# Kernel optimization log

Measured on AMD Instinct MI355X. Metric: run time of the kernel, lower is better.

Reference implementation:

```python
import jax, jax.numpy as jnp
import numpy as np

B, T = 256, 64          # batch, rollout length
D, S, A, E, H = 1024, 64, 32, 1024, 1024  # deter, stoch, action, obs_embed, hidden


def setup_inputs() -> dict:
    key = jax.random.key(0)
    ks = jax.random.split(key, 12)
    f32 = jnp.float32

    def w(k, shape, fan_in):
        return (jax.random.normal(k, shape, f32) / np.float32(np.sqrt(fan_in)))

    return dict(
        obs_embeds=jax.random.normal(ks[0], (B, T, E), f32),
        action_embs=jax.random.normal(ks[1], (B, T, A), f32),
        noise_prior=jax.random.normal(ks[2], (T - 1, B, S), f32),  # randn_like in prior
        noise_post=jax.random.normal(ks[3], (T - 1, B, S), f32),   # randn_like in posterior
        # fc_state_action_embed: Linear(S+A -> D)
        W_sa=w(ks[4], (D, S + A), S + A), b_sa=jnp.zeros((D,), f32),
        # GRUCell(D, D): torch layout [3D, D] with gate order r, z, n
        W_ih=w(ks[5], (3 * D, D), D), b_ih=jnp.zeros((3 * D,), f32),
        W_hh=w(ks[6], (3 * D, D), D), b_hh=jnp.zeros((3 * D,), f32),
        # state_prior: Linear(D->H), ELU, Linear(H->2S)
        Wp1=w(ks[7], (H, D), D), bp1=jnp.zeros((H,), f32),
        Wp2=w(ks[8], (2 * S, H), H), bp2=jnp.zeros((2 * S,), f32),
        # state_posterior: Linear(D+E->H), ELU, Linear(H->2S)
        Wq1=w(ks[9], (H, D + E), D + E), bq1=jnp.zeros((H,), f32),
        Wq2=w(ks[10], (2 * S, H), H), bq2=jnp.zeros((2 * S,), f32),
    )


def reference(obs_embeds, action_embs, noise_prior, noise_post,
              W_sa, b_sa, W_ih, b_ih, W_hh, b_hh,
              Wp1, bp1, Wp2, bp2, Wq1, bq1, Wq2, bq2):
    # observe_rollout: init state is zeros; step t uses obs[:, t+1], action[:, t].
    b = obs_embeds.shape[0]
    h0 = jnp.zeros((b, D), obs_embeds.dtype)
    s0 = jnp.zeros((b, S), obs_embeds.dtype)
    obs_seq = jnp.swapaxes(obs_embeds[:, 1:], 0, 1)   # [T-1, B, E]
    act_seq = jnp.swapaxes(action_embs[:, :-1], 0, 1)  # [T-1, B, A]

    def step(carry, xs):
        h, s = carry  # posterior deter / stoch state from previous step
        obs, act, ep, eq = xs
        # prior: embed (stoch, action) -> GRU update
        e = jax.nn.elu(jnp.concatenate([s, act], -1) @ W_sa.T + b_sa)
        gi = e @ W_ih.T + b_ih
        gh = h @ W_hh.T + b_hh
        ir, iz, ia = jnp.split(gi, 3, axis=-1)
        hr, hz, ha = jnp.split(gh, 3, axis=-1)
        r = jax.nn.sigmoid(ir + hr)
        z = jax.nn.sigmoid(iz + hz)
        n = jnp.tanh(ia + r * ha)
        h_new = (1.0 - z) * n + z * h  # prior deter state
        # prior dist + reparam sample
        pm = jax.nn.elu(h_new @ Wp1.T + bp1) @ Wp2.T + bp2
        pmean, pstd = jnp.split(pm, 2, axis=-1)
        pstd = jax.nn.softplus(pstd) + 0.1
        pstoch = pmean + pstd * ep
        # posterior dist + reparam sample (conditioned on h_new and obs)
        qm = jax.nn.elu(jnp.concatenate([h_new, obs], -1) @ Wq1.T + bq1) @ Wq2.T + bq2
        qmean, qstd = jnp.split(qm, 2, axis=-1)
        qstd = jax.nn.softplus(qstd) + 0.1
        qstoch = qmean + qstd * eq
        out = jnp.concatenate([h_new, pmean, pstd, pstoch, qmean, qstd, qstoch], -1)
        return (h_new, qstoch), out

    _, outs = jax.lax.scan(step, (h0, s0), (obs_seq, act_seq, noise_prior, noise_post))
    # outs: [T-1, B, D + 6S] = (prior deter, prior mean/std/stoch, post mean/std/stoch)
    return outs
```

## Files before the change

### kernel.cpp

```cpp
#include <hip/hip_runtime.h>

typedef __attribute__((ext_vector_type(8))) short short8;
typedef __attribute__((ext_vector_type(4))) float f32x4;

#define OSTEP (256*1408)

#define OFF_WIH  ((size_t)0)
#define OFF_WHH  ((size_t)3145728)
#define OFF_WP1  ((size_t)6291456)
#define OFF_WQ1  ((size_t)7340032)
#define OFF_WP2  ((size_t)9437184)
#define OFF_WQ2  ((size_t)9568256)
#define OFF_HBF0 ((size_t)9699328)
#define OFF_HBF1 ((size_t)9961472)
#define OFF_EBF  ((size_t)10223616)
#define OFF_P1E  ((size_t)10485760)
#define OFF_Q1E  ((size_t)10747904)
#define F32_BYTE_OFF ((size_t)22020096)

__device__ __forceinline__ unsigned short f2bf(float f){
  union { float f; unsigned u; } v; v.f = f;
  unsigned u = v.u;
  u += 0x7fffu + ((u >> 16) & 1u);
  return (unsigned short)(u >> 16);
}
__device__ __forceinline__ float sigf(float x){ return 1.0f/(1.0f+__expf(-x)); }
__device__ __forceinline__ float tanhf_(float x){
  float e = __expf(-2.0f*fabsf(x));
  float t = (1.0f-e)/(1.0f+e);
  return x>=0.f ? t : -t;
}
__device__ __forceinline__ float eluf(float x){ return x>0.f ? x : __expf(x)-1.0f; }
__device__ __forceinline__ float softplusf(float x){ return x>20.f ? x : log1pf(__expf(x)); }
__device__ __forceinline__ short8 ld8(const unsigned short* p){ return *(const short8*)p; }

__global__ void k_prep(const float* __restrict__ wih, const float* __restrict__ whh,
                       const float* __restrict__ wp1, const float* __restrict__ wq1,
                       const float* __restrict__ wp2, const float* __restrict__ wq2,
                       unsigned short* __restrict__ dst){
  size_t i4 = ((size_t)blockIdx.x*256 + threadIdx.x)*4;
  const size_t total = 9699328;
  if(i4 >= total) return;
  const float* src; size_t off;
  if(i4 < 3145728){ src=wih; off=0; }
  else if(i4 < 6291456){ src=whh; off=3145728; }
  else if(i4 < 7340032){ src=wp1; off=6291456; }
  else if(i4 < 9437184){ src=wq1; off=7340032; }
  else if(i4 < 9568256){ src=wp2; off=9437184; }
  else { src=wq2; off=9568256; }
  size_t j = i4 - off;
  float4 v = *(const float4*)(src + j);
  unsigned long long p = (unsigned long long)f2bf(v.x)
                       | ((unsigned long long)f2bf(v.y) << 16)
                       | ((unsigned long long)f2bf(v.z) << 32)
                       | ((unsigned long long)f2bf(v.w) << 48);
  *(unsigned long long*)(dst + i4) = p;
}

__global__ __launch_bounds__(384) void k_gru(
    const unsigned short* __restrict__ e_bf,
    const unsigned short* __restrict__ h_bf,
    const unsigned short* __restrict__ wih_bf,
    const unsigned short* __restrict__ whh_bf,
    const float* __restrict__ b_ih, const float* __restrict__ b_hh,
    const float* __restrict__ hprev, int hprev_ld,
    float* __restrict__ out_t,
    unsigned short* __restrict__ hnext_bf)
{
  int bx = blockIdx.x, by = blockIdx.y;
  int tid = threadIdx.x, w = tid >> 6, lane = tid & 63;
  int g = w % 3; bool isI = (w < 3);
  const unsigned short* A  = isI ? e_bf  : h_bf;
  const unsigned short* Bw = isI ? wih_bf : whh_bf;
  int brow = g*1024 + bx*32;
  int arow = by*32;
  int l15 = lane & 15, q8 = (lane >> 4)*8;

  f32x4 z4 = {0.f,0.f,0.f,0.f};
  f32x4 acc00=z4, acc01=z4, acc10=z4, acc11=z4;

  const unsigned short* pa0 = A  + (size_t)(arow + l15)*1024 + q8;
  const unsigned short* pa1 = pa0 + 16*1024;
  const unsigned short* pb0 = Bw + (size_t)(brow + l15)*1024 + q8;
  const unsigned short* pb1 = pb0 + 16*1024;

  #pragma unroll 4
  for(int kk=0; kk<1024; kk+=32){
    short8 a0 = ld8(pa0+kk), a1 = ld8(pa1+kk);
    short8 b0 = ld8(pb0+kk), b1 = ld8(pb1+kk);
    acc00 = __builtin_amdgcn_mfma_f32_16x16x32_bf16(a0,b0,acc00,0,0,0);
    acc01 = __builtin_amdgcn_mfma_f32_16x16x32_bf16(a0,b1,acc01,0,0,0);
    acc10 = __builtin_amdgcn_mfma_f32_16x16x32_bf16(a1,b0,acc10,0,0,0);
    acc11 = __builtin_amdgcn_mfma_f32_16x16x32_bf16(a1,b1,acc11,0,0,0);
  }

  __shared__ float sg[6][32][33];
  int rr = (lane>>4)*4;
  #pragma unroll
  for(int v=0; v<4; v++){
    sg[w][0 +rr+v][0 +l15] = acc00[v];
    sg[w][0 +rr+v][16+l15] = acc01[v];
    sg[w][16+rr+v][0 +l15] = acc10[v];
    sg[w][16+rr+v][16+l15] = acc11[v];
  }
  __syncthreads();

  for(int i=tid; i<1024; i+=384){
    int m = i>>5, n = i&31;
    int d = bx*32+n, b = by*32+m;
    float ir = sg[0][m][n] + b_ih[d];
    float iz = sg[1][m][n] + b_ih[1024+d];
    float ia = sg[2][m][n] + b_ih[2048+d];
    float hr = sg[3][m][n] + b_hh[d];
    float hz = sg[4][m][n] + b_hh[1024+d];
    float ha = sg[5][m][n] + b_hh[2048+d];
    float r = sigf(ir+hr), zz = sigf(iz+hz);
    float nn = tanhf_(ia + r*ha);
    float hold = hprev[(size_t)b*hprev_ld + d];
    float hnew = (1.f-zz)*nn + zz*hold;
    out_t[(size_t)b*1408 + d] = hnew;
    hnext_bf[(size_t)b*1024 + d] = f2bf(hnew);
  }
}

__global__ __launch_bounds__(256) void k_heads1(
    const unsigned short* __restrict__ hnew_bf,
    const float* __restrict__ obs, int tcol,
    const unsigned short* __restrict__ wp1_bf,
    const unsigned short* __restrict__ wq1_bf,
    const float* __restrict__ bp1, const float* __restrict__ bq1,
    unsigned short* __restrict__ p1e, unsigned short* __restrict__ q1e)
{
  int bx = blockIdx.x, by = blockIdx.y;
  bool isQ = (bx >= 32); int nt = bx & 31;
  int tid = threadIdx.x, w = tid>>6, lane = tid&63;
  int mi = w & 1, ni = w >> 1;
  int l15 = lane & 15, q8 = (lane>>4)*8;
  int arowg = by*32 + mi*16 + l15;
  int browg = nt*32 + ni*16 + l15;

  f32x4 acc = {0.f,0.f,0.f,0.f};
  const unsigned short* pa = hnew_bf + (size_t)arowg*1024 + q8;

  if(!isQ){
    const unsigned short* pb = wp1_bf + (size_t)browg*1024 + q8;
    #pragma unroll 4
    for(int kk=0; kk<1024; kk+=32){
      acc = __builtin_amdgcn_mfma_f32_16x16x32_bf16(ld8(pa+kk), ld8(pb+kk), acc,0,0,0);
    }
  } else {
    const unsigned short* pb = wq1_bf + (size_t)browg*2048 + q8;
    #pragma unroll 4
    for(int kk=0; kk<1024; kk+=32){
      acc = __builtin_amdgcn_mfma_f32_16x16x32_bf16(ld8(pa+kk), ld8(pb+kk), acc,0,0,0);
    }
    const float* obsrow = obs + ((size_t)arowg*64 + tcol)*1024 + q8;
    #pragma unroll 4
    for(int kk=0; kk<1024; kk+=32){
      const float4* f = (const float4*)(obsrow + kk);
      float4 x0 = f[0], x1 = f[1];
      short8 a;
      a[0]=(short)f2bf(x0.x); a[1]=(short)f2bf(x0.y); a[2]=(short)f2bf(x0.z); a[3]=(short)f2bf(x0.w);
      a[4]=(short)f2bf(x1.x); a[5]=(short)f2bf(x1.y); a[6]=(short)f2bf(x1.z); a[7]=(short)f2bf(x1.w);
      acc = __builtin_amdgcn_mfma_f32_16x16x32_bf16(a, ld8(pb+1024+kk), acc,0,0,0);
    }
  }

  const float* bias = isQ ? bq1 : bp1;
  unsigned short* dst = isQ ? q1e : p1e;
  int col = browg;
  float bv = bias[col];
  #pragma unroll
  for(int v=0; v<4; v++){
    int b = by*32 + mi*16 + (lane>>4)*4 + v;
    float val = eluf(acc[v] + bv);
    dst[(size_t)b*1024 + col] = f2bf(val);
  }
}

__global__ __launch_bounds__(256) void k_heads2(
    const unsigned short* __restrict__ p1e, const unsigned short* __restrict__ q1e,
    const unsigned short* __restrict__ wp2_bf, const unsigned short* __restrict__ wq2_bf,
    const float* __restrict__ bp2, const float* __restrict__ bq2,
    float* __restrict__ pm, float* __restrict__ qm)
{
  int bx = blockIdx.x, by = blockIdx.y;
  int col0 = bx*32; bool isQ = (col0 >= 128); int c0 = col0 & 127;
  int tid = threadIdx.x, w = tid>>6, lane = tid&63;
  int mi = w & 1, ni = w >> 1;
  int l15 = lane & 15, q8 = (lane>>4)*8;
  const unsigned short* A  = isQ ? q1e : p1e;
  const unsigned short* Bw = isQ ? wq2_bf : wp2_bf;
  const float* bias = isQ ? bq2 : bp2;
  float* outb = isQ ? qm : pm;

  int arowg = by*32 + mi*16 + l15;
  int browg = c0 + ni*16 + l15;
  f32x4 acc = {0.f,0.f,0.f,0.f};
  const unsigned short* pa = A  + (size_t)arowg*1024 + q8;
  const unsigned short* pb = Bw + (size_t)browg*1024 + q8;
  #pragma unroll 4
  for(int kk=0; kk<1024; kk+=32){
    acc = __builtin_amdgcn_mfma_f32_16x16x32_bf16(ld8(pa+kk), ld8(pb+kk), acc,0,0,0);
  }
  float bv = bias[browg];
  #pragma unroll
  for(int v=0; v<4; v++){
    int b = by*32 + mi*16 + (lane>>4)*4 + v;
    outb[(size_t)b*128 + browg] = acc[v] + bv;
  }
}

__global__ __launch_bounds__(256) void k_sample_e(
    int t_out, int t_act,
    const float* __restrict__ pm, const float* __restrict__ qm,
    const float* __restrict__ noise_p, const float* __restrict__ noise_q,
    const float* __restrict__ act, const float* __restrict__ w_sa,
    const float* __restrict__ b_sa,
    float* __restrict__ out, unsigned short* __restrict__ e_bf)
{
  __shared__ float qst[32*64];
  __shared__ float sact[32*32];
  int bx = blockIdx.x, by = blockIdx.y, tid = threadIdx.x;

  if(t_out >= 0){
    float* out_t = out + (size_t)t_out*OSTEP;
    for(int i=tid; i<2048; i+=256){
      int m = i>>6, s = i&63; int b = by*32+m;
      float qmean = qm[(size_t)b*128 + s];
      float qstd  = softplusf(qm[(size_t)b*128 + 64 + s]) + 0.1f;
      float qs = qmean + qstd * noise_q[((size_t)t_out*256 + b)*64 + s];
      qst[m*64+s] = qs;
      if(bx == 0){
        float pmean = pm[(size_t)b*128 + s];
        float pstd  = softplusf(pm[(size_t)b*128 + 64 + s]) + 0.1f;
        float ps = pmean + pstd * noise_p[((size_t)t_out*256 + b)*64 + s];
        float* o = out_t + (size_t)b*1408;
        o[1024+s] = pmean; o[1088+s] = pstd; o[1152+s] = ps;
        o[1216+s] = qmean; o[1280+s] = qstd; o[1344+s] = qs;
      }
    }
  } else {
    for(int i=tid; i<2048; i+=256) qst[i] = 0.f;
  }
  for(int i=tid; i<1024; i+=256){
    int m = i>>5, k = i&31;
    sact[i] = act[((size_t)(by*32+m)*64 + t_act)*32 + k];
  }
  __syncthreads();

  int n = tid & 31, mb = tid >> 5;
  int d = bx*32 + n;
  const float* wrow = w_sa + (size_t)d*96;
  float a0=b_sa[d], a1=a0, a2=a0, a3=a0;
  for(int k=0; k<64; k++){
    float wv = wrow[k];
    a0 += qst[(mb+ 0)*64+k]*wv;
    a1 += qst[(mb+ 8)*64+k]*wv;
    a2 += qst[(mb+16)*64+k]*wv;
    a3 += qst[(mb+24)*64+k]*wv;
  }
  for(int k=0; k<32; k++){
    float wv = wrow[64+k];
    a0 += sact[(mb+ 0)*32+k]*wv;
    a1 += sact[(mb+ 8)*32+k]*wv;
    a2 += sact[(mb+16)*32+k]*wv;
    a3 += sact[(mb+24)*32+k]*wv;
  }
  e_bf[(size_t)(by*32+mb+ 0)*1024 + d] = f2bf(eluf(a0));
  e_bf[(size_t)(by*32+mb+ 8)*1024 + d] = f2bf(eluf(a1));
  e_bf[(size_t)(by*32+mb+16)*1024 + d] = f2bf(eluf(a2));
  e_bf[(size_t)(by*32+mb+24)*1024 + d] = f2bf(eluf(a3));
}

extern "C" void kernel_launch(void* const* d_in, const int* in_sizes, int n_in,
                              void* d_out, int out_size, void* d_ws, size_t ws_size,
                              hipStream_t stream) {
  const float* obs = (const float*)d_in[0];
  const float* act = (const float*)d_in[1];
  const float* np_ = (const float*)d_in[2];
  const float* nq_ = (const float*)d_in[3];
  const float* wsa = (const float*)d_in[4];
  const float* bsa = (const float*)d_in[5];
  const float* wih = (const float*)d_in[6];
  const float* bih = (const float*)d_in[7];
  const float* whh = (const float*)d_in[8];
  const float* bhh = (const float*)d_in[9];
  const float* wp1 = (const float*)d_in[10];
  const float* bp1 = (const float*)d_in[11];
  const float* wp2 = (const float*)d_in[12];
  const float* bp2 = (const float*)d_in[13];
  const float* wq1 = (const float*)d_in[14];
  const float* bq1 = (const float*)d_in[15];
  const float* wq2 = (const float*)d_in[16];
  const float* bq2 = (const float*)d_in[17];
  float* out = (float*)d_out;

  unsigned short* wsb = (unsigned short*)d_ws;
  unsigned short* wihb = wsb + OFF_WIH;
  unsigned short* whhb = wsb + OFF_WHH;
  unsigned short* wp1b = wsb + OFF_WP1;
  unsigned short* wq1b = wsb + OFF_WQ1;
  unsigned short* wp2b = wsb + OFF_WP2;
  unsigned short* wq2b = wsb + OFF_WQ2;
  unsigned short* hbf0 = wsb + OFF_HBF0;
  unsigned short* hbf1 = wsb + OFF_HBF1;
  unsigned short* ebf  = wsb + OFF_EBF;
  unsigned short* p1e  = wsb + OFF_P1E;
  unsigned short* q1e  = wsb + OFF_Q1E;
  float* f32b = (float*)((char*)d_ws + F32_BYTE_OFF);
  float* h0 = f32b;
  float* pm = f32b + 262144;
  float* qm = f32b + 262144 + 32768;

  hipMemsetAsync(hbf0, 0, 262144*2, stream);
  hipMemsetAsync(h0, 0, 262144*4, stream);

  k_prep<<<9472, 256, 0, stream>>>(wih, whh, wp1, wq1, wp2, wq2, wsb);

  k_sample_e<<<dim3(32,8), 256, 0, stream>>>(-1, 0, pm, qm, np_, nq_, act, wsa, bsa, out, ebf);

  for(int t=0; t<63; t++){
    const unsigned short* hb = (t&1) ? hbf1 : hbf0;
    unsigned short* hbn      = (t&1) ? hbf0 : hbf1;
    const float* hprev = t ? (out + (size_t)(t-1)*OSTEP) : h0;
    int hld = t ? 1408 : 1024;
    k_gru<<<dim3(32,8), 384, 0, stream>>>(ebf, hb, wihb, whhb, bih, bhh,
                                          hprev, hld, out + (size_t)t*OSTEP, hbn);
    k_heads1<<<dim3(64,8), 256, 0, stream>>>(hbn, obs, t+1, wp1b, wq1b, bp1, bq1, p1e, q1e);
    k_heads2<<<dim3(8,8), 256, 0, stream>>>(p1e, q1e, wp2b, wq2b, bp2, bq2, pm, qm);
    k_sample_e<<<dim3(32,8), 256, 0, stream>>>(t, t+1, pm, qm, np_, nq_, act, wsa, bsa, out, ebf);
  }
}
```

Before: 5.991 ms.

## Replace per-step kernel launches with single persistent cooperative kernel using grid syncs

Replaces the prep plus four-kernels-per-timestep launch sequence with one persistent cooperative kernel of 256 blocks that loops over all 63 steps and separates phases with grid.sync. The GRU gates are fused into a single tile pass with all six accumulators per wave, and the obs slice is converted to bf16 once per step. The head-2 output, sampling and the state-action embedding are merged into one phase, with the embedding now done by MFMA in bf16. This removes about 250 kernel launches and the global round-trips for pm/qm, at the cost of grid-wide barriers, idle blocks in the smaller phases, and extra bf16 rounding in the embedding.

```diff
diff --git a/kernel.cpp b/kernel.cpp
--- a/kernel.cpp
+++ b/kernel.cpp
@@ -1,4 +1,7 @@
 #include <hip/hip_runtime.h>
+#include <hip/hip_cooperative_groups.h>
+
+namespace cg = cooperative_groups;
 
 typedef __attribute__((ext_vector_type(8))) short short8;
 typedef __attribute__((ext_vector_type(4))) float f32x4;
@@ -11,12 +14,13 @@
 #define OFF_WQ1  ((size_t)7340032)
 #define OFF_WP2  ((size_t)9437184)
 #define OFF_WQ2  ((size_t)9568256)
-#define OFF_HBF0 ((size_t)9699328)
-#define OFF_HBF1 ((size_t)9961472)
-#define OFF_EBF  ((size_t)10223616)
-#define OFF_P1E  ((size_t)10485760)
-#define OFF_Q1E  ((size_t)10747904)
-#define F32_BYTE_OFF ((size_t)22020096)
+#define OFF_WSA  ((size_t)9699328)
+#define OFF_HBF0 ((size_t)9797632)
+#define OFF_HBF1 ((size_t)10059776)
+#define OFF_EBF  ((size_t)10321920)
+#define OFF_P1E  ((size_t)10584064)
+#define OFF_Q1E  ((size_t)10846208)
+#define OFF_OBSB ((size_t)11108352)
 
 __device__ __forceinline__ unsigned short f2bf(float f){
   union { float f; unsigned u; } v; v.f = f;
@@ -24,6 +28,10 @@
   u += 0x7fffu + ((u >> 16) & 1u);
   return (unsigned short)(u >> 16);
 }
+__device__ __forceinline__ unsigned long long pack4(float4 v){
+  return (unsigned long long)f2bf(v.x) | ((unsigned long long)f2bf(v.y)<<16)
+       | ((unsigned long long)f2bf(v.z)<<32) | ((unsigned long long)f2bf(v.w)<<48);
+}
 __device__ __forceinline__ float sigf(float x){ return 1.0f/(1.0f+__expf(-x)); }
 __device__ __forceinline__ float tanhf_(float x){
   float e = __expf(-2.0f*fabsf(x));
@@ -33,244 +41,210 @@
 __device__ __forceinline__ float eluf(float x){ return x>0.f ? x : __expf(x)-1.0f; }
 __device__ __forceinline__ float softplusf(float x){ return x>20.f ? x : log1pf(__expf(x)); }
 __device__ __forceinline__ short8 ld8(const unsigned short* p){ return *(const short8*)p; }
-
-__global__ void k_prep(const float* __restrict__ wih, const float* __restrict__ whh,
-                       const float* __restrict__ wp1, const float* __restrict__ wq1,
-                       const float* __restrict__ wp2, const float* __restrict__ wq2,
-                       unsigned short* __restrict__ dst){
-  size_t i4 = ((size_t)blockIdx.x*256 + threadIdx.x)*4;
-  const size_t total = 9699328;
-  if(i4 >= total) return;
-  const float* src; size_t off;
-  if(i4 < 3145728){ src=wih; off=0; }
-  else if(i4 < 6291456){ src=whh; off=3145728; }
-  else if(i4 < 7340032){ src=wp1; off=6291456; }
-  else if(i4 < 9437184){ src=wq1; off=7340032; }
-  else if(i4 < 9568256){ src=wp2; off=9437184; }
-  else { src=wq2; off=9568256; }
-  size_t j = i4 - off;
-  float4 v = *(const float4*)(src + j);
-  unsigned long long p = (unsigned long long)f2bf(v.x)
-                       | ((unsigned long long)f2bf(v.y) << 16)
-                       | ((unsigned long long)f2bf(v.z) << 32)
-                       | ((unsigned long long)f2bf(v.w) << 48);
-  *(unsigned long long*)(dst + i4) = p;
-}
-
-__global__ __launch_bounds__(384) void k_gru(
-    const unsigned short* __restrict__ e_bf,
-    const unsigned short* __restrict__ h_bf,
-    const unsigned short* __restrict__ wih_bf,
-    const unsigned short* __restrict__ whh_bf,
-    const float* __restrict__ b_ih, const float* __restrict__ b_hh,
-    const float* __restrict__ hprev, int hprev_ld,
-    float* __restrict__ out_t,
-    unsigned short* __restrict__ hnext_bf)
+__device__ __forceinline__ short8 cvt8(const float* p){
+  short8 r;
+  #pragma unroll
+  for(int i=0;i<8;i++) r[i]=(short)f2bf(p[i]);
+  return r;
+}
+#define MFMA(a,b,c) __builtin_amdgcn_mfma_f32_16x16x32_bf16((a),(b),(c),0,0,0)
+
+__device__ __forceinline__ void e_gemm(int row0, int w, int lane,
+    const float (*sst)[96], const unsigned short* wsab, const float* bsa,
+    unsigned short* ebf){
+  int l15 = lane&15, q8 = (lane>>4)*8, rr = (lane>>4)*4;
+  short8 a0 = cvt8(&sst[l15][q8]);
+  short8 a1 = cvt8(&sst[l15][32+q8]);
+  short8 a2 = cvt8(&sst[l15][64+q8]);
+  #pragma unroll 4
+  for(int n=0;n<16;n++){
+    int col = w*256 + n*16 + l15;
+    const unsigned short* pb = wsab + (size_t)col*96 + q8;
+    f32x4 c = {0.f,0.f,0.f,0.f};
+    c = MFMA(a0, ld8(pb),    c);
+    c = MFMA(a1, ld8(pb+32), c);
+    c = MFMA(a2, ld8(pb+64), c);
+    float bb = bsa[col];
+    #pragma unroll
+    for(int v=0;v<4;v++)
+      ebf[(size_t)(row0+rr+v)*1024 + col] = f2bf(eluf(c[v]+bb));
+  }
+}
+
+__global__ __launch_bounds__(256,1) void k_rssm(
+    const float* __restrict__ obs, const float* __restrict__ act,
+    const float* __restrict__ np_, const float* __restrict__ nq_,
+    const float* __restrict__ wsa_f, const float* __restrict__ bsa,
+    const float* __restrict__ wih_f, const float* __restrict__ bih,
+    const float* __restrict__ whh_f, const float* __restrict__ bhh,
+    const float* __restrict__ wp1_f, const float* __restrict__ bp1,
+    const float* __restrict__ wp2_f, const float* __restrict__ bp2,
+    const float* __restrict__ wq1_f, const float* __restrict__ bq1,
+    const float* __restrict__ wq2_f, const float* __restrict__ bq2,
+    float* __restrict__ out, unsigned short* __restrict__ wsb)
 {
-  int bx = blockIdx.x, by = blockIdx.y;
-  int tid = threadIdx.x, w = tid >> 6, lane = tid & 63;
-  int g = w % 3; bool isI = (w < 3);
-  const unsigned short* A  = isI ? e_bf  : h_bf;
-  const unsigned short* Bw = isI ? wih_bf : whh_bf;
-  int brow = g*1024 + bx*32;
-  int arow = by*32;
-  int l15 = lane & 15, q8 = (lane >> 4)*8;
-
-  f32x4 z4 = {0.f,0.f,0.f,0.f};
-  f32x4 acc00=z4, acc01=z4, acc10=z4, acc11=z4;
-
-  const unsigned short* pa0 = A  + (size_t)(arow + l15)*1024 + q8;
-  const unsigned short* pa1 = pa0 + 16*1024;
-  const unsigned short* pb0 = Bw + (size_t)(brow + l15)*1024 + q8;
-  const unsigned short* pb1 = pb0 + 16*1024;
-
-  #pragma unroll 4
-  for(int kk=0; kk<1024; kk+=32){
-    short8 a0 = ld8(pa0+kk), a1 = ld8(pa1+kk);
-    short8 b0 = ld8(pb0+kk), b1 = ld8(pb1+kk);
-    acc00 = __builtin_amdgcn_mfma_f32_16x16x32_bf16(a0,b0,acc00,0,0,0);
-    acc01 = __builtin_amdgcn_mfma_f32_16x16x32_bf16(a0,b1,acc01,0,0,0);
-    acc10 = __builtin_amdgcn_mfma_f32_16x16x32_bf16(a1,b0,acc10,0,0,0);
-    acc11 = __builtin_amdgcn_mfma_f32_16x16x32_bf16(a1,b1,acc11,0,0,0);
-  }
-
-  __shared__ float sg[6][32][33];
-  int rr = (lane>>4)*4;
-  #pragma unroll
-  for(int v=0; v<4; v++){
-    sg[w][0 +rr+v][0 +l15] = acc00[v];
-    sg[w][0 +rr+v][16+l15] = acc01[v];
-    sg[w][16+rr+v][0 +l15] = acc10[v];
-    sg[w][16+rr+v][16+l15] = acc11[v];
-  }
-  __syncthreads();
-
-  for(int i=tid; i<1024; i+=384){
-    int m = i>>5, n = i&31;
-    int d = bx*32+n, b = by*32+m;
-    float ir = sg[0][m][n] + b_ih[d];
-    float iz = sg[1][m][n] + b_ih[1024+d];
-    float ia = sg[2][m][n] + b_ih[2048+d];
-    float hr = sg[3][m][n] + b_hh[d];
-    float hz = sg[4][m][n] + b_hh[1024+d];
-    float ha = sg[5][m][n] + b_hh[2048+d];
-    float r = sigf(ir+hr), zz = sigf(iz+hz);
-    float nn = tanhf_(ia + r*ha);
-    float hold = hprev[(size_t)b*hprev_ld + d];
-    float hnew = (1.f-zz)*nn + zz*hold;
-    out_t[(size_t)b*1408 + d] = hnew;
-    hnext_bf[(size_t)b*1024 + d] = f2bf(hnew);
-  }
-}
-
-__global__ __launch_bounds__(256) void k_heads1(
-    const unsigned short* __restrict__ hnew_bf,
-    const float* __restrict__ obs, int tcol,
-    const unsigned short* __restrict__ wp1_bf,
-    const unsigned short* __restrict__ wq1_bf,
-    const float* __restrict__ bp1, const float* __restrict__ bq1,
-    unsigned short* __restrict__ p1e, unsigned short* __restrict__ q1e)
-{
-  int bx = blockIdx.x, by = blockIdx.y;
-  bool isQ = (bx >= 32); int nt = bx & 31;
-  int tid = threadIdx.x, w = tid>>6, lane = tid&63;
-  int mi = w & 1, ni = w >> 1;
-  int l15 = lane & 15, q8 = (lane>>4)*8;
-  int arowg = by*32 + mi*16 + l15;
-  int browg = nt*32 + ni*16 + l15;
-
-  f32x4 acc = {0.f,0.f,0.f,0.f};
-  const unsigned short* pa = hnew_bf + (size_t)arowg*1024 + q8;
-
-  if(!isQ){
-    const unsigned short* pb = wp1_bf + (size_t)browg*1024 + q8;
-    #pragma unroll 4
-    for(int kk=0; kk<1024; kk+=32){
-      acc = __builtin_amdgcn_mfma_f32_16x16x32_bf16(ld8(pa+kk), ld8(pb+kk), acc,0,0,0);
-    }
-  } else {
-    const unsigned short* pb = wq1_bf + (size_t)browg*2048 + q8;
-    #pragma unroll 4
-    for(int kk=0; kk<1024; kk+=32){
-      acc = __builtin_amdgcn_mfma_f32_16x16x32_bf16(ld8(pa+kk), ld8(pb+kk), acc,0,0,0);
-    }
-    const float* obsrow = obs + ((size_t)arowg*64 + tcol)*1024 + q8;
-    #pragma unroll 4
-    for(int kk=0; kk<1024; kk+=32){
-      const float4* f = (const float4*)(obsrow + kk);
-      float4 x0 = f[0], x1 = f[1];
-      short8 a;
-      a[0]=(short)f2bf(x0.x); a[1]=(short)f2bf(x0.y); a[2]=(short)f2bf(x0.z); a[3]=(short)f2bf(x0.w);
-      a[4]=(short)f2bf(x1.x); a[5]=(short)f2bf(x1.y); a[6]=(short)f2bf(x1.z); a[7]=(short)f2bf(x1.w);
-      acc = __builtin_amdgcn_mfma_f32_16x16x32_bf16(a, ld8(pb+1024+kk), acc,0,0,0);
-    }
-  }
-
-  const float* bias = isQ ? bq1 : bp1;
-  unsigned short* dst = isQ ? q1e : p1e;
-  int col = browg;
-  float bv = bias[col];
-  #pragma unroll
-  for(int v=0; v<4; v++){
-    int b = by*32 + mi*16 + (lane>>4)*4 + v;
-    float val = eluf(acc[v] + bv);
-    dst[(size_t)b*1024 + col] = f2bf(val);
-  }
-}
-
-__global__ __launch_bounds__(256) void k_heads2(
-    const unsigned short* __restrict__ p1e, const unsigned short* __restrict__ q1e,
-    const unsigned short* __restrict__ wp2_bf, const unsigned short* __restrict__ wq2_bf,
-    const float* __restrict__ bp2, const float* __restrict__ bq2,
-    float* __restrict__ pm, float* __restrict__ qm)
-{
-  int bx = blockIdx.x, by = blockIdx.y;
-  int col0 = bx*32; bool isQ = (col0 >= 128); int c0 = col0 & 127;
-  int tid = threadIdx.x, w = tid>>6, lane = tid&63;
-  int mi = w & 1, ni = w >> 1;
-  int l15 = lane & 15, q8 = (lane>>4)*8;
-  const unsigned short* A  = isQ ? q1e : p1e;
-  const unsigned short* Bw = isQ ? wq2_bf : wp2_bf;
-  const float* bias = isQ ? bq2 : bp2;
-  float* outb = isQ ? qm : pm;
-
-  int arowg = by*32 + mi*16 + l15;
-  int browg = c0 + ni*16 + l15;
-  f32x4 acc = {0.f,0.f,0.f,0.f};
-  const unsigned short* pa = A  + (size_t)arowg*1024 + q8;
-  const unsigned short* pb = Bw + (size_t)browg*1024 + q8;
-  #pragma unroll 4
-  for(int kk=0; kk<1024; kk+=32){
-    acc = __builtin_amdgcn_mfma_f32_16x16x32_bf16(ld8(pa+kk), ld8(pb+kk), acc,0,0,0);
-  }
-  float bv = bias[browg];
-  #pragma unroll
-  for(int v=0; v<4; v++){
-    int b = by*32 + mi*16 + (lane>>4)*4 + v;
-    outb[(size_t)b*128 + browg] = acc[v] + bv;
-  }
-}
-
-__global__ __launch_bounds__(256) void k_sample_e(
-    int t_out, int t_act,
-    const float* __restrict__ pm, const float* __restrict__ qm,
-    const float* __restrict__ noise_p, const float* __restrict__ noise_q,
-    const float* __restrict__ act, const float* __restrict__ w_sa,
-    const float* __restrict__ b_sa,
-    float* __restrict__ out, unsigned short* __restrict__ e_bf)
-{
-  __shared__ float qst[32*64];
-  __shared__ float sact[32*32];
-  int bx = blockIdx.x, by = blockIdx.y, tid = threadIdx.x;
-
-  if(t_out >= 0){
-    float* out_t = out + (size_t)t_out*OSTEP;
-    for(int i=tid; i<2048; i+=256){
-      int m = i>>6, s = i&63; int b = by*32+m;
-      float qmean = qm[(size_t)b*128 + s];
-      float qstd  = softplusf(qm[(size_t)b*128 + 64 + s]) + 0.1f;
-      float qs = qmean + qstd * noise_q[((size_t)t_out*256 + b)*64 + s];
-      qst[m*64+s] = qs;
-      if(bx == 0){
-        float pmean = pm[(size_t)b*128 + s];
-        float pstd  = softplusf(pm[(size_t)b*128 + 64 + s]) + 0.1f;
-        float ps = pmean + pstd * noise_p[((size_t)t_out*256 + b)*64 + s];
-        float* o = out_t + (size_t)b*1408;
-        o[1024+s] = pmean; o[1088+s] = pstd; o[1152+s] = ps;
-        o[1216+s] = qmean; o[1280+s] = qstd; o[1344+s] = qs;
-      }
-    }
-  } else {
-    for(int i=tid; i<2048; i+=256) qst[i] = 0.f;
-  }
-  for(int i=tid; i<1024; i+=256){
-    int m = i>>5, k = i&31;
-    sact[i] = act[((size_t)(by*32+m)*64 + t_act)*32 + k];
-  }
-  __syncthreads();
-
-  int n = tid & 31, mb = tid >> 5;
-  int d = bx*32 + n;
-  const float* wrow = w_sa + (size_t)d*96;
-  float a0=b_sa[d], a1=a0, a2=a0, a3=a0;
-  for(int k=0; k<64; k++){
-    float wv = wrow[k];
-    a0 += qst[(mb+ 0)*64+k]*wv;
-    a1 += qst[(mb+ 8)*64+k]*wv;
-    a2 += qst[(mb+16)*64+k]*wv;
-    a3 += qst[(mb+24)*64+k]*wv;
-  }
-  for(int k=0; k<32; k++){
-    float wv = wrow[64+k];
-    a0 += sact[(mb+ 0)*32+k]*wv;
-    a1 += sact[(mb+ 8)*32+k]*wv;
-    a2 += sact[(mb+16)*32+k]*wv;
-    a3 += sact[(mb+24)*32+k]*wv;
-  }
-  e_bf[(size_t)(by*32+mb+ 0)*1024 + d] = f2bf(eluf(a0));
-  e_bf[(size_t)(by*32+mb+ 8)*1024 + d] = f2bf(eluf(a1));
-  e_bf[(size_t)(by*32+mb+16)*1024 + d] = f2bf(eluf(a2));
-  e_bf[(size_t)(by*32+mb+24)*1024 + d] = f2bf(eluf(a3));
+  cg::grid_group grid = cg::this_grid();
+  const int p = blockIdx.x, tid = threadIdx.x;
+  const int w = tid>>6, lane = tid&63;
+  const int l15 = lane&15, q8 = (lane>>4)*8, rr = (lane>>4)*4;
+  const int gtid = p*256 + tid;
+
+  unsigned short* wihb = wsb + OFF_WIH;
+  unsigned short* whhb = wsb + OFF_WHH;
+  unsigned short* wp1b = wsb + OFF_WP1;
+  unsigned short* wq1b = wsb + OFF_WQ1;
+  unsigned short* wp2b = wsb + OFF_WP2;
+  unsigned short* wq2b = wsb + OFF_WQ2;
+  unsigned short* wsab = wsb + OFF_WSA;
+  unsigned short* ebf  = wsb + OFF_EBF;
+  unsigned short* p1e  = wsb + OFF_P1E;
+  unsigned short* q1e  = wsb + OFF_Q1E;
+  unsigned short* obsb = wsb + OFF_OBSB;
+
+  __shared__ float sm[16][130];
+  __shared__ float sst[16][96];
+
+  {
+    const float* srcs[7] = {wih_f, whh_f, wp1_f, wq1_f, wp2_f, wq2_f, wsa_f};
+    const size_t offs[7] = {OFF_WIH, OFF_WHH, OFF_WP1, OFF_WQ1, OFF_WP2, OFF_WQ2, OFF_WSA};
+    const size_t cnts[7] = {3145728,3145728,1048576,2097152,131072,131072,98304};
+    #pragma unroll 1
+    for(int s=0;s<7;s++){
+      const float4* src = (const float4*)srcs[s];
+      unsigned long long* dst = (unsigned long long*)(wsb + offs[s]);
+      size_t n4 = cnts[s] >> 2;
+      for(size_t i=gtid; i<n4; i+=65536) dst[i] = pack4(src[i]);
+    }
+    unsigned long long* hz = (unsigned long long*)(wsb + OFF_HBF0);
+    hz[gtid] = 0ull;
+  }
+  grid.sync();
+
+  if(p < 16){
+    int row0 = p*16;
+    for(int i=tid;i<16*96;i+=256) (&sst[0][0])[i] = 0.f;
+    __syncthreads();
+    for(int i=tid;i<512;i+=256){ int r=i>>5, a2=i&31;
+      sst[r][64+a2] = act[((size_t)(row0+r)*64 + 0)*32 + a2]; }
+    __syncthreads();
+    e_gemm(row0, w, lane, sst, wsab, bsa, ebf);
+  }
+  grid.sync();
+
+  for(int t=0;t<63;t++){
+    const unsigned short* hb  = (t&1) ? wsb+OFF_HBF1 : wsb+OFF_HBF0;
+    unsigned short*       hbn = (t&1) ? wsb+OFF_HBF0 : wsb+OFF_HBF1;
+    float* out_t = out + (size_t)t*OSTEP;
+
+    {
+      int j = p>>2, m = p&3;
+      int row0 = m*64 + w*16;
+      const unsigned short* pe = ebf + (size_t)(row0+l15)*1024 + q8;
+      const unsigned short* ph = hb  + (size_t)(row0+l15)*1024 + q8;
+      int d = j*16 + l15;
+      const unsigned short* pwi = wihb + (size_t)d*1024 + q8;
+      const unsigned short* pwh = whhb + (size_t)d*1024 + q8;
+      f32x4 z4 = {0.f,0.f,0.f,0.f};
+      f32x4 aIR=z4, aIZ=z4, aIA=z4, aHR=z4, aHZ=z4, aHA=z4;
+      #pragma unroll 2
+      for(int k=0;k<1024;k+=32){
+        short8 ae = ld8(pe+k), ah = ld8(ph+k);
+        aIR = MFMA(ae, ld8(pwi+k),         aIR);
+        aIZ = MFMA(ae, ld8(pwi+1048576+k), aIZ);
+        aIA = MFMA(ae, ld8(pwi+2097152+k), aIA);
+        aHR = MFMA(ah, ld8(pwh+k),         aHR);
+        aHZ = MFMA(ah, ld8(pwh+1048576+k), aHZ);
+        aHA = MFMA(ah, ld8(pwh+2097152+k), aHA);
+      }
+      float bir=bih[d], biz=bih[1024+d], bia=bih[2048+d];
+      float bhr=bhh[d], bhz=bhh[1024+d], bha=bhh[2048+d];
+      #pragma unroll
+      for(int v=0;v<4;v++){
+        int b = row0 + rr + v;
+        float r  = sigf(aIR[v]+bir + aHR[v]+bhr);
+        float zz = sigf(aIZ[v]+biz + aHZ[v]+bhz);
+        float nn = tanhf_(aIA[v]+bia + r*(aHA[v]+bha));
+        float hold = (t==0) ? 0.f : out[(size_t)(t-1)*OSTEP + (size_t)b*1408 + d];
+        float hnew = (1.f-zz)*nn + zz*hold;
+        out_t[(size_t)b*1408 + d] = hnew;
+        hbn[(size_t)b*1024 + d] = f2bf(hnew);
+      }
+      int bo = gtid>>8, e4 = (gtid&255)*4;
+      float4 v = *(const float4*)(obs + ((size_t)bo*64 + (t+1))*1024 + e4);
+      *(unsigned long long*)(obsb + (size_t)bo*1024 + e4) = pack4(v);
+    }
+    grid.sync();
+
+    {
+      int j = p>>2, m = p&3;
+      int row0 = m*64 + w*16;
+      const unsigned short* pa = hbn  + (size_t)(row0+l15)*1024 + q8;
+      const unsigned short* po = obsb + (size_t)(row0+l15)*1024 + q8;
+      int hc = j*16 + l15;
+      const unsigned short* pbp = wp1b + (size_t)hc*1024 + q8;
+      const unsigned short* pbq = wq1b + (size_t)hc*2048 + q8;
+      f32x4 z4 = {0.f,0.f,0.f,0.f};
+      f32x4 ap=z4, aq=z4, ao=z4;
+      #pragma unroll 2
+      for(int k=0;k<1024;k+=32){
+        short8 a = ld8(pa+k), o = ld8(po+k);
+        ap = MFMA(a, ld8(pbp+k),      ap);
+        aq = MFMA(a, ld8(pbq+k),      aq);
+        ao = MFMA(o, ld8(pbq+1024+k), ao);
+      }
+      float bp = bp1[hc], bq = bq1[hc];
+      #pragma unroll
+      for(int v=0;v<4;v++){
+        int b = row0 + rr + v;
+        p1e[(size_t)b*1024 + hc] = f2bf(eluf(ap[v]+bp));
+        q1e[(size_t)b*1024 + hc] = f2bf(eluf(aq[v]+ao[v]+bq));
+      }
+    }
+    grid.sync();
+
+    if(p < 32){
+      bool isQ = (p < 16);
+      int row0 = (p&15)*16;
+      const unsigned short* A  = isQ ? q1e : p1e;
+      const unsigned short* W2 = isQ ? wq2b : wp2b;
+      const float* b2 = isQ ? bq2 : bp2;
+      const unsigned short* pa  = A  + (size_t)(row0+l15)*1024 + q8;
+      const unsigned short* pb0 = W2 + (size_t)(w*32+l15)*1024 + q8;
+      const unsigned short* pb1 = pb0 + (size_t)16*1024;
+      f32x4 c0 = {0.f,0.f,0.f,0.f}, c1 = c0;
+      #pragma unroll 2
+      for(int k=0;k<1024;k+=32){
+        short8 a = ld8(pa+k);
+        c0 = MFMA(a, ld8(pb0+k), c0);
+        c1 = MFMA(a, ld8(pb1+k), c1);
+      }
+      int cb = w*32 + l15;
+      #pragma unroll
+      for(int v=0;v<4;v++){
+        sm[rr+v][cb]    = c0[v] + b2[cb];
+        sm[rr+v][cb+16] = c1[v] + b2[cb+16];
+      }
+      __syncthreads();
+      const float* noise = isQ ? nq_ : np_;
+      int obase = isQ ? 1216 : 1024;
+      for(int i=tid;i<1024;i+=256){
+        int r=i>>6, s=i&63; int b=row0+r;
+        float mean = sm[r][s];
+        float stdv = softplusf(sm[r][64+s]) + 0.1f;
+        float samp = mean + stdv * noise[((size_t)t*256 + b)*64 + s];
+        float* o = out_t + (size_t)b*1408 + obase;
+        o[s]=mean; o[64+s]=stdv; o[128+s]=samp;
+        if(isQ) sst[r][s] = samp;
+      }
+      if(isQ){
+        for(int i=tid;i<512;i+=256){ int r=i>>5, a2=i&31;
+          sst[r][64+a2] = act[((size_t)(row0+r)*64 + (t+1))*32 + a2]; }
+      }
+      __syncthreads();
+      if(isQ) e_gemm(row0, w, lane, sst, wsab, bsa, ebf);
+    }
+    grid.sync();
+  }
 }
 
 extern "C" void kernel_launch(void* const* d_in, const int* in_sizes, int n_in,
@@ -295,40 +269,14 @@
   const float* wq2 = (const float*)d_in[16];
   const float* bq2 = (const float*)d_in[17];
   float* out = (float*)d_out;
-
   unsigned short* wsb = (unsigned short*)d_ws;
-  unsigned short* wihb = wsb + OFF_WIH;
-  unsigned short* whhb = wsb + OFF_WHH;
-  unsigned short* wp1b = wsb + OFF_WP1;
-  unsigned short* wq1b = wsb + OFF_WQ1;
-  unsigned short* wp2b = wsb + OFF_WP2;
-  unsigned short* wq2b = wsb + OFF_WQ2;
-  unsigned short* hbf0 = wsb + OFF_HBF0;
-  unsigned short* hbf1 = wsb + OFF_HBF1;
-  unsigned short* ebf  = wsb + OFF_EBF;
-  unsigned short* p1e  = wsb + OFF_P1E;
-  unsigned short* q1e  = wsb + OFF_Q1E;
-  float* f32b = (float*)((char*)d_ws + F32_BYTE_OFF);
-  float* h0 = f32b;
-  float* pm = f32b + 262144;
-  float* qm = f32b + 262144 + 32768;
-
-  hipMemsetAsync(hbf0, 0, 262144*2, stream);
-  hipMemsetAsync(h0, 0, 262144*4, stream);
-
-  k_prep<<<9472, 256, 0, stream>>>(wih, whh, wp1, wq1, wp2, wq2, wsb);
-
-  k_sample_e<<<dim3(32,8), 256, 0, stream>>>(-1, 0, pm, qm, np_, nq_, act, wsa, bsa, out, ebf);
-
-  for(int t=0; t<63; t++){
-    const unsigned short* hb = (t&1) ? hbf1 : hbf0;
-    unsigned short* hbn      = (t&1) ? hbf0 : hbf1;
-    const float* hprev = t ? (out + (size_t)(t-1)*OSTEP) : h0;
-    int hld = t ? 1408 : 1024;
-    k_gru<<<dim3(32,8), 384, 0, stream>>>(ebf, hb, wihb, whhb, bih, bhh,
-                                          hprev, hld, out + (size_t)t*OSTEP, hbn);
-    k_heads1<<<dim3(64,8), 256, 0, stream>>>(hbn, obs, t+1, wp1b, wq1b, bp1, bq1, p1e, q1e);
-    k_heads2<<<dim3(8,8), 256, 0, stream>>>(p1e, q1e, wp2b, wq2b, bp2, bq2, pm, qm);
-    k_sample_e<<<dim3(32,8), 256, 0, stream>>>(t, t+1, pm, qm, np_, nq_, act, wsa, bsa, out, ebf);
-  }
-}
+
+  void* args[] = {
+    (void*)&obs, (void*)&act, (void*)&np_, (void*)&nq_,
+    (void*)&wsa, (void*)&bsa, (void*)&wih, (void*)&bih,
+    (void*)&whh, (void*)&bhh, (void*)&wp1, (void*)&bp1,
+    (void*)&wp2, (void*)&bp2, (void*)&wq1, (void*)&bq1,
+    (void*)&wq2, (void*)&bq2, (void*)&out, (void*)&wsb
+  };
+  hipLaunchCooperativeKernel((const void*)k_rssm, dim3(256), dim3(256), args, 0, stream);
+}
```

Result: slower. 9.767 ms (+63.0%).
